# Performance work log

Measured on AMD Instinct MI355X. Metric: run time of the kernel, lower is better.

The kernel has to match this reference:

```python
import jax, jax.numpy as jnp
import numpy as np

NC, S, T, F, D, A = 617, 200000, 15, 5, 64, 768
E, EC, L = 1000000, 20000, 2


def setup_inputs():
    key = jax.random.key(0)
    ks = jax.random.split(key, 24)
    f = jnp.float32
    sc = 0.08
    return {
        "company_ts": jax.random.normal(ks[0], (NC, T, F), f),
        "sentence_x": jax.random.normal(ks[1], (S, A), f),
        "company_ids": jnp.arange(NC, dtype=jnp.int32),
        "ei_c2c_src": jax.random.randint(ks[2], (EC,), 0, NC),
        "ei_c2c_dst": jax.random.randint(ks[3], (EC,), 0, NC),
        "ei_s2c_src": jax.random.randint(ks[4], (E,), 0, S),
        "ei_s2c_dst": jax.random.randint(ks[5], (E,), 0, NC),
        "ei_c2s_src": jax.random.randint(ks[6], (E,), 0, NC),
        "ei_c2s_dst": jax.random.randint(ks[7], (E,), 0, S),
        "bn_gamma": jnp.ones((T,), f),
        "bn_beta": jnp.zeros((T,), f),
        "lstm_Wih0": sc * jax.random.normal(ks[8], (4 * D, 1), f),
        "lstm_Whh0": sc * jax.random.normal(ks[9], (4 * D, D), f),
        "lstm_bih0": jnp.zeros((4 * D,), f),
        "lstm_bhh0": jnp.zeros((4 * D,), f),
        "lstm_Wih1": sc * jax.random.normal(ks[10], (4 * D, D), f),
        "lstm_Whh1": sc * jax.random.normal(ks[11], (4 * D, D), f),
        "lstm_bih1": jnp.zeros((4 * D,), f),
        "lstm_bhh1": jnp.zeros((4 * D,), f),
        "fc_W": sc * jax.random.normal(ks[12], (D, D), f),
        "fc_b": jnp.zeros((D,), f),
        "comp_emb": jax.random.normal(ks[13], (NC, D), f),
        "proj_W": sc * jax.random.normal(ks[14], (D, A), f),
        "proj_b": jnp.zeros((D,), f),
        "gin_W": sc * jax.random.normal(ks[15], (L, 3, D, D), f),
        "gin_b": jnp.zeros((L, 3, D), f),
        "gin_a": 0.25 * jnp.ones((L, 3), f),  # PReLU slope, torch default init
        "cls_W": sc * jax.random.normal(ks[16], (2, D), f),
        "cls_b": jnp.zeros((2,), f),
    }


def _lstm_layer(x, Wih, Whh, bih, bhh):
    # x: [N, T, I] -> [N, T, H]; torch gate order i, f, g, o
    N = x.shape[0]
    H = Whh.shape[1]

    def step(carry, xt):
        h, c = carry
        g = xt @ Wih.T + h @ Whh.T + bih + bhh
        i, fg, gg, o = jnp.split(g, 4, axis=-1)
        c = jax.nn.sigmoid(fg) * c + jax.nn.sigmoid(i) * jnp.tanh(gg)
        h = jax.nn.sigmoid(o) * jnp.tanh(c)
        return (h, c), h

    init = (jnp.zeros((N, H), x.dtype), jnp.zeros((N, H), x.dtype))
    _, hs = jax.lax.scan(step, init, jnp.swapaxes(x, 0, 1))
    return jnp.swapaxes(hs, 0, 1)


def _gin(x_src, x_dst, src, dst, n_dst, W, b, a):
    # GINConv(eps=0), nn = Linear + PReLU: prelu(W @ (x_dst + sum_{e->i} x_src[src_e]) + b)
    msg = jax.ops.segment_sum(x_src[src], dst, num_segments=n_dst)
    h = (x_dst + msg) @ W.T + b
    return jnp.where(h >= 0, h, a * h)


def reference(company_ts, sentence_x, company_ids, ei_c2c_src, ei_c2c_dst,
              ei_s2c_src, ei_s2c_dst, ei_c2s_src, ei_c2s_dst,
              bn_gamma, bn_beta, lstm_Wih0, lstm_Whh0, lstm_bih0, lstm_bhh0,
              lstm_Wih1, lstm_Whh1, lstm_bih1, lstm_bhh1, fc_W, fc_b,
              comp_emb, proj_W, proj_b, gin_W, gin_b, gin_a, cls_W, cls_b):
    # LSTM branch on the second-to-last timeseries feature
    ts = company_ts[:, :, -2:-1]                       # [NC, T, 1]
    mean = ts.mean(axis=(0, 2), keepdims=True)         # BatchNorm1d(T), training stats
    var = ts.var(axis=(0, 2), keepdims=True)
    ts = (ts - mean) / jnp.sqrt(var + 1e-5)
    ts = ts * bn_gamma[None, :, None] + bn_beta[None, :, None]
    h = _lstm_layer(ts, lstm_Wih0, lstm_Whh0, lstm_bih0, lstm_bhh0)
    h = _lstm_layer(h, lstm_Wih1, lstm_Whh1, lstm_bih1, lstm_bhh1)
    comp_ts = jax.nn.relu(h[:, -1, :] @ fc_W.T + fc_b)  # [NC, D]

    # node features: company = lstm + embedding; sentence = projected article emb
    comp = comp_ts + comp_emb[company_ids]
    sent = sentence_x @ proj_W.T + proj_b               # [S, D]

    # to_hetero(GConv): per-edge-type GINConv, sum-aggregate over edge types per dst type
    n_comp, n_sent = comp.shape[0], sent.shape[0]
    for l in range(gin_W.shape[0]):
        new_comp = (_gin(comp, comp, ei_c2c_src, ei_c2c_dst, n_comp,
                         gin_W[l, 0], gin_b[l, 0], gin_a[l, 0])
                    + _gin(sent, comp, ei_s2c_src, ei_s2c_dst, n_comp,
                           gin_W[l, 1], gin_b[l, 1], gin_a[l, 1]))
        new_sent = _gin(comp, sent, ei_c2s_src, ei_c2s_dst, n_sent,
                        gin_W[l, 2], gin_b[l, 2], gin_a[l, 2])
        comp, sent = new_comp, new_sent

    return comp @ cls_W.T + cls_b                       # [NC, 2]
```

## Files before the change

### kernel.cpp

```cpp
#include <hip/hip_runtime.h>

#define NCC 617
#define TTT 15
#define FFF 5
#define SSN 200000
#define EEN 1000000
#define ECN 20000
#define CSBLK 196
#define NB2 512
#define EPB2 ((EEN + NB2 - 1) / NB2)
#define ZN (NCC + NCC + SSN + SSN)

typedef unsigned short u16;
typedef unsigned int   u32;

using short8  = __attribute__((ext_vector_type(8))) short;
using f32x4v  = __attribute__((ext_vector_type(4))) float;

__device__ __forceinline__ float bf2f(u16 u){ return __uint_as_float(((u32)u) << 16); }
__device__ __forceinline__ u16 f2bf(float f){
  u32 x = __float_as_uint(f);
  u32 r = (x + 0x7fffu + ((x >> 16) & 1u)) >> 16;
  return (u16)r;
}
__device__ __forceinline__ u32 pk2(float a, float b){ return (u32)f2bf(a) | ((u32)f2bf(b) << 16); }
__device__ __forceinline__ float sigm(float x){ return 1.0f / (1.0f + __expf(-x)); }

__global__ __launch_bounds__(256) void k_hist2z(const int* __restrict__ dst, int* __restrict__ blockHist,
                                                int* __restrict__ cntBase){
  __shared__ int h[NCC];
  int b = blockIdx.x, tid = threadIdx.x;
  const int zper = (ZN + NB2 - 1) / NB2;
  for (int i = tid; i < zper; i += 256){
    int gi = b * zper + i;
    if (gi < ZN) cntBase[gi] = 0;
  }
  for (int i = tid; i < NCC; i += 256) h[i] = 0;
  __syncthreads();
  int e0 = b * EPB2;
  int e1 = e0 + EPB2; if (e1 > EEN) e1 = EEN;
  for (int e = e0 + tid; e < e1; e += 256) atomicAdd(&h[dst[e]], 1);
  __syncthreads();
  for (int i = tid; i < NCC; i += 256) blockHist[i * NB2 + b] = h[i];
}

__global__ __launch_bounds__(256) void k_hist_all(const int* d1, int n1, int* c1,
                                                  const int* d2, int n2, int* c2){
  int i = blockIdx.x * 256 + threadIdx.x;
  if (i < n1) atomicAdd(&c1[d1[i]], 1);
  else if (i < n1 + n2) atomicAdd(&c2[d2[i - n1]], 1);
}

__global__ __launch_bounds__(64) void k_colscan(int* __restrict__ blockHist, int* __restrict__ colTotal){
  int d = blockIdx.x, lane = threadIdx.x;
  int base = 0;
  for (int j = 0; j < NB2; j += 64){
    int v = blockHist[d * NB2 + j + lane];
    int orig = v;
    #pragma unroll
    for (int s = 1; s < 64; s <<= 1){
      int t = __shfl_up(v, s, 64);
      if (lane >= s) v += t;
    }
    blockHist[d * NB2 + j + lane] = base + v - orig;
    base += __shfl(v, 63, 64);
  }
  if (lane == 0) colTotal[d] = base;
}

__global__ __launch_bounds__(1024) void k_scan2(const int* cntA, int* ofsA,
                                                const int* cntB, int* ofsB, int n){
  __shared__ int buf[1024];
  int t = threadIdx.x;
  for (int pass = 0; pass < 2; ++pass){
    const int* cnt = pass ? cntB : cntA;
    int* ofs = pass ? ofsB : ofsA;
    int v = (t < n) ? cnt[t] : 0;
    buf[t] = v;
    __syncthreads();
    for (int d = 1; d < 1024; d <<= 1){
      int x = (t >= d) ? buf[t - d] : 0;
      __syncthreads();
      buf[t] += x;
      __syncthreads();
    }
    if (t < n) ofs[t] = (t == 0) ? 0 : buf[t - 1];
    if (t == 0) ofs[n] = buf[n - 1];
    __syncthreads();
  }
}

__global__ __launch_bounds__(1024) void k_scan_blocks(const int* cnt, int* ofs, int n, int* bsum){
  __shared__ int buf[1024];
  int t = threadIdx.x;
  int gi = blockIdx.x * 1024 + t;
  int v = (gi < n) ? cnt[gi] : 0;
  buf[t] = v;
  __syncthreads();
  for (int d = 1; d < 1024; d <<= 1){
    int x = (t >= d) ? buf[t - d] : 0;
    __syncthreads();
    buf[t] += x;
    __syncthreads();
  }
  if (gi < n) ofs[gi] = buf[t] - v;
  if (t == 1023) bsum[blockIdx.x] = buf[1023];
}

__global__ __launch_bounds__(1024) void k_scan_addB(int* __restrict__ ofs, const int* __restrict__ bsum, int n){
  __shared__ int sboff[CSBLK + 1];
  int tid = threadIdx.x, lane = tid & 63;
  if (tid < 64){
    int base = 0;
    for (int j = 0; j < CSBLK; j += 64){
      int idx = j + lane;
      int v = (idx < CSBLK) ? bsum[idx] : 0;
      int orig = v;
      #pragma unroll
      for (int s = 1; s < 64; s <<= 1){
        int t2 = __shfl_up(v, s, 64);
        if (lane >= s) v += t2;
      }
      if (idx < CSBLK) sboff[idx] = base + v - orig;
      base += __shfl(v, 63, 64);
    }
    if (lane == 0) sboff[CSBLK] = base;
  }
  __syncthreads();
  int gi = blockIdx.x * 1024 + tid;
  if (gi < n) ofs[gi] += sboff[blockIdx.x];
  if (blockIdx.x == 0 && tid == 0) ofs[n] = sboff[CSBLK];
}

__global__ __launch_bounds__(256) void k_scatter2(const int* __restrict__ src, const int* __restrict__ dst,
                                                  const int* __restrict__ blockHist, const int* __restrict__ off,
                                                  int* __restrict__ bkt){
  __shared__ int cur[NCC];
  int b = blockIdx.x, tid = threadIdx.x;
  for (int i = tid; i < NCC; i += 256) cur[i] = off[i] + blockHist[i * NB2 + b];
  __syncthreads();
  int e0 = b * EPB2;
  int e1 = e0 + EPB2; if (e1 > EEN) e1 = EEN;
  for (int e = e0 + tid; e < e1; e += 256){
    int d = dst[e];
    int p = atomicAdd(&cur[d], 1);
    bkt[p] = src[e];
  }
}

__global__ __launch_bounds__(256) void k_scatter_all(const int* s1, const int* d1, const int* off1, int* cnt1, int* bkt1, int n1,
                                                     const int* s2, const int* d2, const int* off2, int* cnt2, int* bkt2, int n2){
  int i = blockIdx.x * 256 + threadIdx.x;
  if (i < n1){
    int d = d1[i]; int p = off1[d] + atomicAdd(&cnt1[d], 1); bkt1[p] = s1[i];
  } else if (i < n1 + n2){
    int k = i - n1;
    int d = d2[k]; int p = off2[d] + atomicAdd(&cnt2[d], 1); bkt2[p] = s2[k];
  }
}

__global__ __launch_bounds__(256) void k_bn(const float* ts, const float* gamma, const float* beta, float* outp){
  __shared__ float ss[256], s2[256];
  int t = blockIdx.x, tid = threadIdx.x;
  float a = 0.f, b = 0.f;
  for (int c = tid; c < NCC; c += 256){
    float v = ts[(c * TTT + t) * FFF + 3];
    a += v; b += v * v;
  }
  ss[tid] = a; s2[tid] = b;
  __syncthreads();
  for (int d = 128; d > 0; d >>= 1){
    if (tid < d){ ss[tid] += ss[tid + d]; s2[tid] += s2[tid + d]; }
    __syncthreads();
  }
  float mean = ss[0] / (float)NCC;
  float var  = s2[0] / (float)NCC - mean * mean;
  float rstd = rsqrtf(var + 1e-5f);
  float g = gamma[t], be = beta[t];
  for (int c = tid; c < NCC; c += 256){
    float v = ts[(c * TTT + t) * FFF + 3];
    outp[c * TTT + t] = (v - mean) * rstd * g + be;
  }
}

__global__ __launch_bounds__(256) void k_lstm0(const float* tsn, const float* Wih0, const float* Whh0,
                                               const float* bih0, const float* bhh0, float* h0seq){
  __shared__ __align__(16) u16 sW[64 * 256];
  __shared__ float sWi[256];
  __shared__ float sB[256];
  int tid = threadIdx.x;
  for (int i = tid; i < 64 * 256; i += 256){
    int j = i >> 6, k = i & 63;
    sW[k * 256 + j] = f2bf(Whh0[i]);
  }
  if (tid < 256){ sWi[tid] = Wih0[tid]; sB[tid] = bih0[tid] + bhh0[tid]; }
  __syncthreads();
  int wave = tid >> 6, lane = tid & 63;
  int c = blockIdx.x * 4 + wave;
  if (c >= NCC) return;
  float wi_i = sWi[lane], wi_f = sWi[64 + lane], wi_g = sWi[128 + lane], wi_o = sWi[192 + lane];
  float b_i = sB[lane], b_f = sB[64 + lane], b_g = sB[128 + lane], b_o = sB[192 + lane];
  float h = 0.f, cs = 0.f;
  for (int t = 0; t < TTT; ++t){
    float x = tsn[c * TTT + t];
    float gi = b_i + x * wi_i, gf = b_f + x * wi_f, gg = b_g + x * wi_g, go = b_o + x * wi_o;
    #pragma unroll 4
    for (int k = 0; k < 64; ++k){
      float hk = __shfl(h, k, 64);
      const u16* w = &sW[k * 256 + lane];
      gi += hk * bf2f(w[0]);
      gf += hk * bf2f(w[64]);
      gg += hk * bf2f(w[128]);
      go += hk * bf2f(w[192]);
    }
    cs = sigm(gf) * cs + sigm(gi) * tanhf(gg);
    h  = sigm(go) * tanhf(cs);
    h0seq[(c * TTT + t) * 64 + lane] = h;
  }
}

__global__ __launch_bounds__(256, 1) void k_lstm1(const float* h0seq, const float* Wih1, const float* Whh1,
                                                  const float* bih1, const float* bhh1,
                                                  const float* fcW, const float* fcb,
                                                  const float* emb, const int* ids, float* comp0){
  __shared__ __align__(16) u16 sWi[64 * 256];
  __shared__ __align__(16) u16 sWh[64 * 256];
  int tid = threadIdx.x;
  for (int i = tid; i < 64 * 256; i += 256){
    int j = i >> 6, k = i & 63;
    sWi[k * 256 + j] = f2bf(Wih1[i]);
    sWh[k * 256 + j] = f2bf(Whh1[i]);
  }
  __syncthreads();
  int wave = tid >> 6, lane = tid & 63;
  int c = blockIdx.x * 4 + wave;
  int ci = (c < NCC) ? c : (NCC - 1);
  float b_i = bih1[lane]        + bhh1[lane];
  float b_f = bih1[64 + lane]   + bhh1[64 + lane];
  float b_g = bih1[128 + lane]  + bhh1[128 + lane];
  float b_o = bih1[192 + lane]  + bhh1[192 + lane];
  float h = 0.f, cs = 0.f;
  for (int t = 0; t < TTT; ++t){
    float x = h0seq[(ci * TTT + t) * 64 + lane];
    float gi = b_i, gf = b_f, gg = b_g, go = b_o;
    #pragma unroll 4
    for (int k = 0; k < 64; ++k){
      float xk = __shfl(x, k, 64);
      float hk = __shfl(h, k, 64);
      const u16* wi = &sWi[k * 256 + lane];
      const u16* wh = &sWh[k * 256 + lane];
      gi += xk * bf2f(wi[0])   + hk * bf2f(wh[0]);
      gf += xk * bf2f(wi[64])  + hk * bf2f(wh[64]);
      gg += xk * bf2f(wi[128]) + hk * bf2f(wh[128]);
      go += xk * bf2f(wi[192]) + hk * bf2f(wh[192]);
    }
    cs = sigm(gf) * cs + sigm(gi) * tanhf(gg);
    h  = sigm(go) * tanhf(cs);
  }
  __syncthreads();
  float* fws = (float*)sWi;
  for (int i = tid; i < 64 * 64; i += 256){
    int d = i >> 6, k = i & 63;
    fws[k * 64 + d] = fcW[i];
  }
  __syncthreads();
  float y = fcb[lane];
  #pragma unroll 4
  for (int k = 0; k < 64; ++k){
    float hk = __shfl(h, k, 64);
    y += hk * fws[k * 64 + lane];
  }
  y = fmaxf(y, 0.f);
  if (c < NCC) comp0[c * 64 + lane] = y + emb[ids[c] * 64 + lane];
}

__global__ __launch_bounds__(256) void k_projm(const float* __restrict__ A, const float* __restrict__ W,
                                               const float* __restrict__ pb, u16* __restrict__ sent0){
  __shared__ __align__(16) u16 sA[128 * 64];
  __shared__ __align__(16) u16 sB[64 * 64];
  char* sAb = (char*)sA;
  char* sBb = (char*)sB;
  int tid = threadIdx.x;
  int wave = tid >> 6, lane = tid & 63;
  int l15 = lane & 15, lg = lane >> 4;
  int s0 = blockIdx.x * 128;

  int rA = tid >> 1, hA = tid & 1;
  int sA_row = s0 + rA; if (sA_row >= SSN) sA_row = SSN - 1;
  const float* gA0 = &A[(size_t)sA_row * 768 + hA * 32];
  u32 aw_base = (u32)(rA * 128 + hA * 64);
  u32 aw_swz  = (u32)((rA & 7) << 4);
  int nB = tid >> 2, qB = tid & 3;
  const float* gB0 = &W[(size_t)nB * 768 + qB * 16];
  u32 bw_base = (u32)(nB * 128 + qB * 32);
  u32 bw_swz  = (u32)((nB & 7) << 4);

  int arow = wave * 32 + l15;
  u32 ar_swz = (u32)((arow & 7) << 4);
  u32 ar_base = (u32)(arow * 128 + lg * 16);
  u32 br_swz = (u32)((l15 & 7) << 4);
  u32 br_base = (u32)(l15 * 128 + lg * 16);

  f32x4v acc[2][4] = {};

  for (int kc = 0; kc < 12; ++kc){
    __syncthreads();
    {
      const float* g = gA0 + kc * 64;
      #pragma unroll
      for (int q = 0; q < 4; ++q){
        float4 va = ((const float4*)g)[2 * q];
        float4 vb = ((const float4*)g)[2 * q + 1];
        uint4 w;
        w.x = pk2(va.x, va.y); w.y = pk2(va.z, va.w);
        w.z = pk2(vb.x, vb.y); w.w = pk2(vb.z, vb.w);
        *(uint4*)(sAb + ((aw_base + q * 16) ^ aw_swz)) = w;
      }
    }
    {
      const float* g = gB0 + kc * 64;
      #pragma unroll
      for (int q = 0; q < 2; ++q){
        float4 va = ((const float4*)g)[2 * q];
        float4 vb = ((const float4*)g)[2 * q + 1];
        uint4 w;
        w.x = pk2(va.x, va.y); w.y = pk2(va.z, va.w);
        w.z = pk2(vb.x, vb.y); w.w = pk2(vb.z, vb.w);
        *(uint4*)(sBb + ((bw_base + q * 16) ^ bw_swz)) = w;
      }
    }
    __syncthreads();
    #pragma unroll
    for (int ks = 0; ks < 2; ++ks){
      short8 a0 = *(const short8*)(sAb + ((ar_base + 0    + ks * 64) ^ ar_swz));
      short8 a1 = *(const short8*)(sAb + ((ar_base + 2048 + ks * 64) ^ ar_swz));
      short8 b0 = *(const short8*)(sBb + ((br_base + 0    + ks * 64) ^ br_swz));
      short8 b1 = *(const short8*)(sBb + ((br_base + 2048 + ks * 64) ^ br_swz));
      short8 b2 = *(const short8*)(sBb + ((br_base + 4096 + ks * 64) ^ br_swz));
      short8 b3 = *(const short8*)(sBb + ((br_base + 6144 + ks * 64) ^ br_swz));
      acc[0][0] = __builtin_amdgcn_mfma_f32_16x16x32_bf16(a0, b0, acc[0][0], 0, 0, 0);
      acc[0][1] = __builtin_amdgcn_mfma_f32_16x16x32_bf16(a0, b1, acc[0][1], 0, 0, 0);
      acc[0][2] = __builtin_amdgcn_mfma_f32_16x16x32_bf16(a0, b2, acc[0][2], 0, 0, 0);
      acc[0][3] = __builtin_amdgcn_mfma_f32_16x16x32_bf16(a0, b3, acc[0][3], 0, 0, 0);
      acc[1][0] = __builtin_amdgcn_mfma_f32_16x16x32_bf16(a1, b0, acc[1][0], 0, 0, 0);
      acc[1][1] = __builtin_amdgcn_mfma_f32_16x16x32_bf16(a1, b1, acc[1][1], 0, 0, 0);
      acc[1][2] = __builtin_amdgcn_mfma_f32_16x16x32_bf16(a1, b2, acc[1][2], 0, 0, 0);
      acc[1][3] = __builtin_amdgcn_mfma_f32_16x16x32_bf16(a1, b3, acc[1][3], 0, 0, 0);
    }
  }

  float bias[4];
  #pragma unroll
  for (int nt = 0; nt < 4; ++nt) bias[nt] = pb[nt * 16 + l15];
  #pragma unroll
  for (int mt = 0; mt < 2; ++mt){
    #pragma unroll
    for (int j = 0; j < 4; ++j){
      int s = s0 + wave * 32 + mt * 16 + lg * 4 + j;
      if (s < SSN){
        #pragma unroll
        for (int nt = 0; nt < 4; ++nt)
          sent0[(size_t)s * 64 + nt * 16 + l15] = f2bf(acc[mt][nt][j] + bias[nt]);
      }
    }
  }
}

__global__ __launch_bounds__(256) void k_sgin(const u16* __restrict__ sentIn, const float* __restrict__ compIn,
                                              const int* __restrict__ ofs, const int* __restrict__ bkt,
                                              const float* __restrict__ W, const float* __restrict__ b,
                                              const float* __restrict__ aP, u16* __restrict__ sentOut){
  __shared__ __align__(16) float Wt[64 * 68];
  __shared__ __align__(16) float Xt[64 * 68];
  __shared__ int eb[512];
  __shared__ int sofs[65];
  int tid = threadIdx.x;
  for (int i = tid; i < 4096; i += 256){
    int j = i >> 6, k = i & 63;
    Wt[k * 68 + j] = W[i];
  }
  int sBase = blockIdx.x * 64;
  if (tid < 65) sofs[tid] = ofs[sBase + tid];
  __syncthreads();
  int E0 = sofs[0];
  int tot = sofs[64] - E0;
  int staged = tot < 512 ? tot : 512;
  for (int i = tid; i < staged; i += 256) eb[i] = bkt[E0 + i];
  __syncthreads();
  int wave = tid >> 6, lane = tid & 63;
  for (int q = 0; q < 16; ++q){
    int sL = wave * 16 + q;
    int s = sBase + sL;
    float acc = bf2f(sentIn[(size_t)s * 64 + lane]);
    int e0 = sofs[sL], e1 = sofs[sL + 1];
    for (int e = e0; e < e1; ++e){
      int r = e - E0;
      int src = (r < 512) ? eb[r] : bkt[e];
      acc += compIn[src * 64 + lane];
    }
    Xt[lane * 68 + sL] = acc;
  }
  __syncthreads();
  int n0 = (tid & 15) * 4, sG = (tid >> 4) * 4;
  float acc[4][4] = {};
  #pragma unroll 4
  for (int k = 0; k < 64; ++k){
    float4 a4 = *(const float4*)&Xt[k * 68 + sG];
    float4 w4 = *(const float4*)&Wt[k * 68 + n0];
    float a_[4] = {a4.x, a4.y, a4.z, a4.w};
    float w_[4] = {w4.x, w4.y, w4.z, w4.w};
    #pragma unroll
    for (int i = 0; i < 4; ++i)
      #pragma unroll
      for (int j = 0; j < 4; ++j)
        acc[i][j] += a_[i] * w_[j];
  }
  float alpha = *aP;
  float4 bv = *(const float4*)&b[n0];
  float b_[4] = {bv.x, bv.y, bv.z, bv.w};
  __syncthreads();
  #pragma unroll
  for (int i = 0; i < 4; ++i){
    ushort4 o;
    #pragma unroll
    for (int j = 0; j < 4; ++j){
      float h = acc[i][j] + b_[j];
      h = (h >= 0.f) ? h : alpha * h;
      ((u16*)&o)[j] = f2bf(h);
    }
    *(ushort4*)&sentOut[(size_t)(sBase + sG + i) * 64 + n0] = o;
  }
}

__global__ __launch_bounds__(1024) void k_cgin(const float* __restrict__ compIn, const u16* __restrict__ sentIn,
                                               const int* __restrict__ ofsA, const int* __restrict__ bktA,
                                               const int* __restrict__ ofsB, const int* __restrict__ bktB,
                                               const float* __restrict__ Wa, const float* __restrict__ ba, const float* aaP,
                                               const float* __restrict__ Wb, const float* __restrict__ bb, const float* abP,
                                               float* __restrict__ compOut,
                                               const float* __restrict__ clsW, const float* __restrict__ clsb,
                                               float* __restrict__ outp){
  __shared__ __align__(16) float Wat[64 * 68];
  __shared__ __align__(16) float Wbt[64 * 68];
  __shared__ int eidx[2048];
  __shared__ float part[16][2][64];
  __shared__ float xa[64], xb[64], outab[128];
  int tid = threadIdx.x;
  for (int i = tid; i < 4096; i += 1024){
    int j = i >> 6, k = i & 63;
    Wat[k * 68 + j] = Wa[i];
    Wbt[k * 68 + j] = Wb[i];
  }
  int wave = tid >> 6, lane = tid & 63;
  int c = blockIdx.x;
  float accA = 0.f, accB = 0.f;
  int a0 = ofsA[c], a1 = ofsA[c + 1];
  for (int base = a0; base < a1; base += 2048){
    int cnt = a1 - base; if (cnt > 2048) cnt = 2048;
    __syncthreads();
    for (int i = tid; i < cnt; i += 1024) eidx[i] = bktA[base + i];
    __syncthreads();
    for (int i = wave; i < cnt; i += 16) accA += compIn[eidx[i] * 64 + lane];
  }
  int b0 = ofsB[c], b1 = ofsB[c + 1];
  for (int base = b0; base < b1; base += 2048){
    int cnt = b1 - base; if (cnt > 2048) cnt = 2048;
    __syncthreads();
    for (int i = tid; i < cnt; i += 1024) eidx[i] = bktB[base + i];
    __syncthreads();
    #pragma unroll 4
    for (int i = wave; i < cnt; i += 16) accB += bf2f(sentIn[(size_t)eidx[i] * 64 + lane]);
  }
  part[wave][0][lane] = accA;
  part[wave][1][lane] = accB;
  __syncthreads();
  if (tid < 128){
    int l = tid & 63, which = tid >> 6;
    float m = 0.f;
    #pragma unroll
    for (int w = 0; w < 16; ++w) m += part[w][which][l];
    float ci = compIn[c * 64 + l];
    if (which == 0) xa[l] = ci + m; else xb[l] = ci + m;
  }
  __syncthreads();
  if (tid < 128){
    int j = tid & 63;
    const float* X  = (tid < 64) ? xa : xb;
    const float* Wt = (tid < 64) ? Wat : Wbt;
    float acc = (tid < 64) ? ba[j] : bb[j];
    #pragma unroll 4
    for (int k = 0; k < 64; ++k) acc += X[k] * Wt[k * 68 + j];
    float al = (tid < 64) ? *aaP : *abP;
    outab[tid] = (acc >= 0.f) ? acc : al * acc;
  }
  __syncthreads();
  if (clsW){
    if (tid < 64) xa[tid] = outab[tid] + outab[64 + tid];
    __syncthreads();
    if (tid < 128){
      int j = tid >> 6;
      float p = xa[lane] * clsW[j * 64 + lane];
      #pragma unroll
      for (int s = 32; s > 0; s >>= 1) p += __shfl_down(p, s, 64);
      if (lane == 0) outp[c * 2 + j] = p + clsb[j];
    }
  } else {
    if (tid < 64) compOut[c * 64 + tid] = outab[tid] + outab[64 + tid];
  }
}

extern "C" void kernel_launch(void* const* d_in, const int* in_sizes, int n_in,
                              void* d_out, int out_size, void* d_ws, size_t ws_size,
                              hipStream_t stream) {
  (void)in_sizes; (void)n_in; (void)out_size; (void)ws_size;
  const float* company_ts = (const float*)d_in[0];
  const float* sentence_x = (const float*)d_in[1];
  const int*   company_ids = (const int*)d_in[2];
  const int*   c2c_src = (const int*)d_in[3];
  const int*   c2c_dst = (const int*)d_in[4];
  const int*   s2c_src = (const int*)d_in[5];
  const int*   s2c_dst = (const int*)d_in[6];
  const int*   c2s_src = (const int*)d_in[7];
  const int*   c2s_dst = (const int*)d_in[8];
  const float* bn_gamma = (const float*)d_in[9];
  const float* bn_beta  = (const float*)d_in[10];
  const float* Wih0 = (const float*)d_in[11];
  const float* Whh0 = (const float*)d_in[12];
  const float* bih0 = (const float*)d_in[13];
  const float* bhh0 = (const float*)d_in[14];
  const float* Wih1 = (const float*)d_in[15];
  const float* Whh1 = (const float*)d_in[16];
  const float* bih1 = (const float*)d_in[17];
  const float* bhh1 = (const float*)d_in[18];
  const float* fc_W = (const float*)d_in[19];
  const float* fc_b = (const float*)d_in[20];
  const float* comp_emb = (const float*)d_in[21];
  const float* proj_W = (const float*)d_in[22];
  const float* proj_b = (const float*)d_in[23];
  const float* gin_W = (const float*)d_in[24];
  const float* gin_b = (const float*)d_in[25];
  const float* gin_a = (const float*)d_in[26];
  const float* cls_W = (const float*)d_in[27];
  const float* cls_b = (const float*)d_in[28];
  float* outp = (float*)d_out;

  char* ws = (char*)d_ws;
  size_t off = 0;
  auto alloc = [&](size_t bytes)->char* {
    char* r = ws + off;
    off += (bytes + 255) & ~(size_t)255;
    return r;
  };
  float* ts_norm = (float*)alloc((size_t)NCC * TTT * 4);
  float* h0seq   = (float*)alloc((size_t)NCC * TTT * 64 * 4);
  float* comp0   = (float*)alloc((size_t)NCC * 64 * 4);
  float* comp1   = (float*)alloc((size_t)NCC * 64 * 4);
  u16*   sent0   = (u16*)alloc((size_t)SSN * 64 * 2);
  int*   blockHist = (int*)alloc((size_t)NCC * NB2 * 4);
  int*   colTotal  = (int*)alloc((size_t)NCC * 4);
  int*   cnt_c2c  = (int*)alloc((size_t)ZN * 4);
  int*   cnt2_c2c = cnt_c2c + NCC;
  int*   cnt_c2s  = cnt2_c2c + NCC;
  int*   cnt2_c2s = cnt_c2s + SSN;
  int*   off_c2c = (int*)alloc((size_t)(NCC + 1) * 4);
  int*   off_s2c = (int*)alloc((size_t)(NCC + 1) * 4);
  int*   off_c2s = (int*)alloc((size_t)(SSN + 1) * 4);
  int*   bkt_c2c = (int*)alloc((size_t)ECN * 4);
  int*   bkt_s2c = (int*)alloc((size_t)EEN * 4);
  int*   bkt_c2s = (int*)alloc((size_t)EEN * 4);
  int*   bsum    = (int*)alloc(256 * 4);

  k_hist2z<<<NB2, 256, 0, stream>>>(s2c_dst, blockHist, cnt_c2c);
  k_hist_all<<<(ECN + EEN + 255) / 256, 256, 0, stream>>>(c2c_dst, ECN, cnt_c2c, c2s_dst, EEN, cnt_c2s);
  k_colscan<<<NCC, 64, 0, stream>>>(blockHist, colTotal);
  k_scan2<<<1, 1024, 0, stream>>>(cnt_c2c, off_c2c, colTotal, off_s2c, NCC);
  k_scan_blocks<<<CSBLK, 1024, 0, stream>>>(cnt_c2s, off_c2s, SSN, bsum);
  k_scan_addB<<<CSBLK, 1024, 0, stream>>>(off_c2s, bsum, SSN);
  k_scatter2<<<NB2, 256, 0, stream>>>(s2c_src, s2c_dst, blockHist, off_s2c, bkt_s2c);
  k_scatter_all<<<(ECN + EEN + 255) / 256, 256, 0, stream>>>(
      c2c_src, c2c_dst, off_c2c, cnt2_c2c, bkt_c2c, ECN,
      c2s_src, c2s_dst, off_c2s, cnt2_c2s, bkt_c2s, EEN);

  k_bn<<<TTT, 256, 0, stream>>>(company_ts, bn_gamma, bn_beta, ts_norm);
  k_lstm0<<<(NCC + 3) / 4, 256, 0, stream>>>(ts_norm, Wih0, Whh0, bih0, bhh0, h0seq);
  k_lstm1<<<(NCC + 3) / 4, 256, 0, stream>>>(h0seq, Wih1, Whh1, bih1, bhh1, fc_W, fc_b,
                                             comp_emb, company_ids, comp0);

  k_projm<<<(SSN + 127) / 128, 256, 0, stream>>>(sentence_x, proj_W, proj_b, sent0);

  k_cgin<<<NCC, 1024, 0, stream>>>(comp0, sent0,
                                   off_c2c, bkt_c2c, off_s2c, bkt_s2c,
                                   gin_W + 0 * 4096, gin_b + 0 * 64, gin_a + 0,
                                   gin_W + 1 * 4096, gin_b + 1 * 64, gin_a + 1,
                                   comp1, nullptr, nullptr, nullptr);
  k_sgin<<<SSN / 64, 256, 0, stream>>>(sent0, comp0, off_c2s, bkt_c2s,
                                       gin_W + 2 * 4096, gin_b + 2 * 64, gin_a + 2,
                                       sent0 );

  k_cgin<<<NCC, 1024, 0, stream>>>(comp1, sent0,
                                   off_c2c, bkt_c2c, off_s2c, bkt_s2c,
                                   gin_W + 3 * 4096, gin_b + 3 * 64, gin_a + 3,
                                   gin_W + 4 * 4096, gin_b + 4 * 64, gin_a + 4,
                                   nullptr, cls_W, cls_b, outp);
}
```

Baseline: 687.1 us.

## Fuse CSR build kernels, merge LSTM layers, and use MFMA in sentence GIN

Combines the histogram, scan and scatter launches into fewer multi-role kernels and folds batch-norm into a scan kernel, cutting launch count and serialization. Fuses the two LSTM layers into one kernel with gate-interleaved bf16 weights for vector LDS loads, which removes the h0seq round trip through global memory. Replaces the fp32 FMA tile GEMM in the sentence GIN with bf16 MFMA on swizzled LDS. The GIN inputs are now rounded to bf16 before the GEMM, and the fused LSTM kernel needs more LDS per block.

```diff
diff --git a/kernel.cpp b/kernel.cpp
--- a/kernel.cpp
+++ b/kernel.cpp
@@ -10,6 +10,7 @@
 #define NB2 512
 #define EPB2 ((EEN + NB2 - 1) / NB2)
 #define ZN (NCC + NCC + SSN + SSN)
+#define HALLB ((ECN + EEN + 255) / 256)
 
 typedef unsigned short u16;
 typedef unsigned int   u32;
@@ -26,240 +27,239 @@
 __device__ __forceinline__ u32 pk2(float a, float b){ return (u32)f2bf(a) | ((u32)f2bf(b) << 16); }
 __device__ __forceinline__ float sigm(float x){ return 1.0f / (1.0f + __expf(-x)); }
 
-__global__ __launch_bounds__(256) void k_hist2z(const int* __restrict__ dst, int* __restrict__ blockHist,
-                                                int* __restrict__ cntBase){
+__global__ __launch_bounds__(256) void k_zero(int* p, int n){
+  int i = blockIdx.x * 256 + threadIdx.x;
+  if (i < n) p[i] = 0;
+}
+
+__global__ __launch_bounds__(256) void k_histF(const int* __restrict__ s2c_dst, int* __restrict__ blockHist,
+                                               const int* __restrict__ c2c_dst, int* __restrict__ cnt_c2c,
+                                               const int* __restrict__ c2s_dst, int* __restrict__ cnt_c2s){
   __shared__ int h[NCC];
   int b = blockIdx.x, tid = threadIdx.x;
-  const int zper = (ZN + NB2 - 1) / NB2;
-  for (int i = tid; i < zper; i += 256){
-    int gi = b * zper + i;
-    if (gi < ZN) cntBase[gi] = 0;
-  }
-  for (int i = tid; i < NCC; i += 256) h[i] = 0;
-  __syncthreads();
-  int e0 = b * EPB2;
-  int e1 = e0 + EPB2; if (e1 > EEN) e1 = EEN;
-  for (int e = e0 + tid; e < e1; e += 256) atomicAdd(&h[dst[e]], 1);
-  __syncthreads();
-  for (int i = tid; i < NCC; i += 256) blockHist[i * NB2 + b] = h[i];
-}
-
-__global__ __launch_bounds__(256) void k_hist_all(const int* d1, int n1, int* c1,
-                                                  const int* d2, int n2, int* c2){
-  int i = blockIdx.x * 256 + threadIdx.x;
-  if (i < n1) atomicAdd(&c1[d1[i]], 1);
-  else if (i < n1 + n2) atomicAdd(&c2[d2[i - n1]], 1);
-}
-
-__global__ __launch_bounds__(64) void k_colscan(int* __restrict__ blockHist, int* __restrict__ colTotal){
-  int d = blockIdx.x, lane = threadIdx.x;
-  int base = 0;
-  for (int j = 0; j < NB2; j += 64){
-    int v = blockHist[d * NB2 + j + lane];
-    int orig = v;
-    #pragma unroll
-    for (int s = 1; s < 64; s <<= 1){
-      int t = __shfl_up(v, s, 64);
-      if (lane >= s) v += t;
-    }
-    blockHist[d * NB2 + j + lane] = base + v - orig;
-    base += __shfl(v, 63, 64);
-  }
-  if (lane == 0) colTotal[d] = base;
-}
-
-__global__ __launch_bounds__(1024) void k_scan2(const int* cntA, int* ofsA,
-                                                const int* cntB, int* ofsB, int n){
+  if (b < NB2){
+    for (int i = tid; i < NCC; i += 256) h[i] = 0;
+    __syncthreads();
+    int e0 = b * EPB2;
+    int e1 = e0 + EPB2; if (e1 > EEN) e1 = EEN;
+    for (int e = e0 + tid; e < e1; e += 256) atomicAdd(&h[s2c_dst[e]], 1);
+    __syncthreads();
+    for (int i = tid; i < NCC; i += 256) blockHist[i * NB2 + b] = h[i];
+  } else {
+    int i = (b - NB2) * 256 + tid;
+    if (i < ECN) atomicAdd(&cnt_c2c[c2c_dst[i]], 1);
+    else if (i < ECN + EEN) atomicAdd(&cnt_c2s[c2s_dst[i - ECN]], 1);
+  }
+}
+
+__global__ __launch_bounds__(1024) void k_scanA(int* __restrict__ blockHist, int* __restrict__ colTotal,
+                                                const int* __restrict__ cnt_c2s, int* __restrict__ off_c2s,
+                                                int* __restrict__ bsum,
+                                                const float* __restrict__ ts, const float* __restrict__ gamma,
+                                                const float* __restrict__ beta, float* __restrict__ tsn){
   __shared__ int buf[1024];
-  int t = threadIdx.x;
-  for (int pass = 0; pass < 2; ++pass){
-    const int* cnt = pass ? cntB : cntA;
-    int* ofs = pass ? ofsB : ofsA;
-    int v = (t < n) ? cnt[t] : 0;
-    buf[t] = v;
+  __shared__ float ss[1024], s2[1024];
+  int b = blockIdx.x, tid = threadIdx.x;
+  if (b < NCC){
+    if (tid < 64){
+      int lane = tid;
+      int base = 0;
+      for (int j = 0; j < NB2; j += 64){
+        int v = blockHist[b * NB2 + j + lane];
+        int orig = v;
+        #pragma unroll
+        for (int s = 1; s < 64; s <<= 1){
+          int t = __shfl_up(v, s, 64);
+          if (lane >= s) v += t;
+        }
+        blockHist[b * NB2 + j + lane] = base + v - orig;
+        base += __shfl(v, 63, 64);
+      }
+      if (lane == 0) colTotal[b] = base;
+    }
+  } else if (b < NCC + CSBLK) {
+    int bb = b - NCC;
+    int gi = bb * 1024 + tid;
+    int v = (gi < SSN) ? cnt_c2s[gi] : 0;
+    buf[tid] = v;
     __syncthreads();
     for (int d = 1; d < 1024; d <<= 1){
-      int x = (t >= d) ? buf[t - d] : 0;
+      int x = (tid >= d) ? buf[tid - d] : 0;
       __syncthreads();
-      buf[t] += x;
+      buf[tid] += x;
       __syncthreads();
     }
-    if (t < n) ofs[t] = (t == 0) ? 0 : buf[t - 1];
-    if (t == 0) ofs[n] = buf[n - 1];
-    __syncthreads();
-  }
-}
-
-__global__ __launch_bounds__(1024) void k_scan_blocks(const int* cnt, int* ofs, int n, int* bsum){
+    if (gi < SSN) off_c2s[gi] = buf[tid] - v;
+    if (tid == 1023) bsum[bb] = buf[1023];
+  } else {
+    int t = b - (NCC + CSBLK);
+    float a = 0.f, s = 0.f;
+    for (int c = tid; c < NCC; c += 1024){
+      float v = ts[(c * TTT + t) * FFF + 3];
+      a += v; s += v * v;
+    }
+    ss[tid] = a; s2[tid] = s;
+    __syncthreads();
+    for (int d = 512; d > 0; d >>= 1){
+      if (tid < d){ ss[tid] += ss[tid + d]; s2[tid] += s2[tid + d]; }
+      __syncthreads();
+    }
+    float mean = ss[0] / (float)NCC;
+    float var  = s2[0] / (float)NCC - mean * mean;
+    float rstd = rsqrtf(var + 1e-5f);
+    float g = gamma[t], be = beta[t];
+    for (int c = tid; c < NCC; c += 1024){
+      float v = ts[(c * TTT + t) * FFF + 3];
+      tsn[c * TTT + t] = (v - mean) * rstd * g + be;
+    }
+  }
+}
+
+__global__ __launch_bounds__(1024) void k_scanB(const int* __restrict__ cnt_c2c, int* __restrict__ off_c2c,
+                                                const int* __restrict__ colTotal, int* __restrict__ off_s2c,
+                                                int* __restrict__ off_c2s, const int* __restrict__ bsum){
   __shared__ int buf[1024];
-  int t = threadIdx.x;
-  int gi = blockIdx.x * 1024 + t;
-  int v = (gi < n) ? cnt[gi] : 0;
-  buf[t] = v;
-  __syncthreads();
-  for (int d = 1; d < 1024; d <<= 1){
-    int x = (t >= d) ? buf[t - d] : 0;
-    __syncthreads();
-    buf[t] += x;
-    __syncthreads();
-  }
-  if (gi < n) ofs[gi] = buf[t] - v;
-  if (t == 1023) bsum[blockIdx.x] = buf[1023];
-}
-
-__global__ __launch_bounds__(1024) void k_scan_addB(int* __restrict__ ofs, const int* __restrict__ bsum, int n){
   __shared__ int sboff[CSBLK + 1];
-  int tid = threadIdx.x, lane = tid & 63;
-  if (tid < 64){
-    int base = 0;
-    for (int j = 0; j < CSBLK; j += 64){
-      int idx = j + lane;
-      int v = (idx < CSBLK) ? bsum[idx] : 0;
-      int orig = v;
-      #pragma unroll
-      for (int s = 1; s < 64; s <<= 1){
-        int t2 = __shfl_up(v, s, 64);
-        if (lane >= s) v += t2;
+  int b = blockIdx.x, tid = threadIdx.x;
+  if (b == 0){
+    for (int pass = 0; pass < 2; ++pass){
+      const int* cnt = pass ? colTotal : cnt_c2c;
+      int* ofs = pass ? off_s2c : off_c2c;
+      int v = (tid < NCC) ? cnt[tid] : 0;
+      buf[tid] = v;
+      __syncthreads();
+      for (int d = 1; d < 1024; d <<= 1){
+        int x = (tid >= d) ? buf[tid - d] : 0;
+        __syncthreads();
+        buf[tid] += x;
+        __syncthreads();
       }
-      if (idx < CSBLK) sboff[idx] = base + v - orig;
-      base += __shfl(v, 63, 64);
-    }
-    if (lane == 0) sboff[CSBLK] = base;
-  }
-  __syncthreads();
-  int gi = blockIdx.x * 1024 + tid;
-  if (gi < n) ofs[gi] += sboff[blockIdx.x];
-  if (blockIdx.x == 0 && tid == 0) ofs[n] = sboff[CSBLK];
-}
-
-__global__ __launch_bounds__(256) void k_scatter2(const int* __restrict__ src, const int* __restrict__ dst,
-                                                  const int* __restrict__ blockHist, const int* __restrict__ off,
-                                                  int* __restrict__ bkt){
+      if (tid < NCC) ofs[tid] = (tid == 0) ? 0 : buf[tid - 1];
+      if (tid == 0) ofs[NCC] = buf[NCC - 1];
+      __syncthreads();
+    }
+  } else {
+    int bb = b - 1;
+    int lane = tid & 63;
+    if (tid < 64){
+      int base = 0;
+      for (int j = 0; j < CSBLK; j += 64){
+        int idx = j + lane;
+        int v = (idx < CSBLK) ? bsum[idx] : 0;
+        int orig = v;
+        #pragma unroll
+        for (int s = 1; s < 64; s <<= 1){
+          int t2 = __shfl_up(v, s, 64);
+          if (lane >= s) v += t2;
+        }
+        if (idx < CSBLK) sboff[idx] = base + v - orig;
+        base += __shfl(v, 63, 64);
+      }
+      if (lane == 0) sboff[CSBLK] = base;
+    }
+    __syncthreads();
+    int gi = bb * 1024 + tid;
+    if (gi < SSN) off_c2s[gi] += sboff[bb];
+    if (bb == 0 && tid == 0) off_c2s[SSN] = sboff[CSBLK];
+  }
+}
+
+__global__ __launch_bounds__(256) void k_scatF(const int* __restrict__ s2c_src, const int* __restrict__ s2c_dst,
+                                               const int* __restrict__ blockHist, const int* __restrict__ off_s2c,
+                                               int* __restrict__ bkt_s2c,
+                                               const int* __restrict__ c2c_src, const int* __restrict__ c2c_dst,
+                                               const int* __restrict__ off_c2c, int* __restrict__ cnt2_c2c,
+                                               int* __restrict__ bkt_c2c,
+                                               const int* __restrict__ c2s_src, const int* __restrict__ c2s_dst,
+                                               const int* __restrict__ off_c2s, int* __restrict__ cnt2_c2s,
+                                               int* __restrict__ bkt_c2s){
   __shared__ int cur[NCC];
   int b = blockIdx.x, tid = threadIdx.x;
-  for (int i = tid; i < NCC; i += 256) cur[i] = off[i] + blockHist[i * NB2 + b];
-  __syncthreads();
-  int e0 = b * EPB2;
-  int e1 = e0 + EPB2; if (e1 > EEN) e1 = EEN;
-  for (int e = e0 + tid; e < e1; e += 256){
-    int d = dst[e];
-    int p = atomicAdd(&cur[d], 1);
-    bkt[p] = src[e];
-  }
-}
-
-__global__ __launch_bounds__(256) void k_scatter_all(const int* s1, const int* d1, const int* off1, int* cnt1, int* bkt1, int n1,
-                                                     const int* s2, const int* d2, const int* off2, int* cnt2, int* bkt2, int n2){
-  int i = blockIdx.x * 256 + threadIdx.x;
-  if (i < n1){
-    int d = d1[i]; int p = off1[d] + atomicAdd(&cnt1[d], 1); bkt1[p] = s1[i];
-  } else if (i < n1 + n2){
-    int k = i - n1;
-    int d = d2[k]; int p = off2[d] + atomicAdd(&cnt2[d], 1); bkt2[p] = s2[k];
-  }
-}
-
-__global__ __launch_bounds__(256) void k_bn(const float* ts, const float* gamma, const float* beta, float* outp){
-  __shared__ float ss[256], s2[256];
-  int t = blockIdx.x, tid = threadIdx.x;
-  float a = 0.f, b = 0.f;
-  for (int c = tid; c < NCC; c += 256){
-    float v = ts[(c * TTT + t) * FFF + 3];
-    a += v; b += v * v;
-  }
-  ss[tid] = a; s2[tid] = b;
-  __syncthreads();
-  for (int d = 128; d > 0; d >>= 1){
-    if (tid < d){ ss[tid] += ss[tid + d]; s2[tid] += s2[tid + d]; }
-    __syncthreads();
-  }
-  float mean = ss[0] / (float)NCC;
-  float var  = s2[0] / (float)NCC - mean * mean;
-  float rstd = rsqrtf(var + 1e-5f);
-  float g = gamma[t], be = beta[t];
-  for (int c = tid; c < NCC; c += 256){
-    float v = ts[(c * TTT + t) * FFF + 3];
-    outp[c * TTT + t] = (v - mean) * rstd * g + be;
-  }
-}
-
-__global__ __launch_bounds__(256) void k_lstm0(const float* tsn, const float* Wih0, const float* Whh0,
-                                               const float* bih0, const float* bhh0, float* h0seq){
-  __shared__ __align__(16) u16 sW[64 * 256];
+  if (b < NB2){
+    for (int i = tid; i < NCC; i += 256) cur[i] = off_s2c[i] + blockHist[i * NB2 + b];
+    __syncthreads();
+    int e0 = b * EPB2;
+    int e1 = e0 + EPB2; if (e1 > EEN) e1 = EEN;
+    for (int e = e0 + tid; e < e1; e += 256){
+      int d = s2c_dst[e];
+      int p = atomicAdd(&cur[d], 1);
+      bkt_s2c[p] = s2c_src[e];
+    }
+  } else {
+    int i = (b - NB2) * 256 + tid;
+    if (i < ECN){
+      int d = c2c_dst[i]; int p = off_c2c[d] + atomicAdd(&cnt2_c2c[d], 1); bkt_c2c[p] = c2c_src[i];
+    } else if (i < ECN + EEN){
+      int k = i - ECN;
+      int d = c2s_dst[k]; int p = off_c2s[d] + atomicAdd(&cnt2_c2s[d], 1); bkt_c2s[p] = c2s_src[k];
+    }
+  }
+}
+
+__global__ __launch_bounds__(256, 1) void k_lstm01(const float* __restrict__ tsn,
+                                                   const float* __restrict__ Wih0, const float* __restrict__ Whh0,
+                                                   const float* __restrict__ bih0, const float* __restrict__ bhh0,
+                                                   const float* __restrict__ Wih1, const float* __restrict__ Whh1,
+                                                   const float* __restrict__ bih1, const float* __restrict__ bhh1,
+                                                   const float* __restrict__ fcW, const float* __restrict__ fcb,
+                                                   const float* __restrict__ emb, const int* __restrict__ ids,
+                                                   float* __restrict__ comp0){
+  __shared__ __align__(16) u16 sW0[64 * 64 * 4];
+  __shared__ __align__(16) u16 sP1[64 * 64 * 8];
   __shared__ float sWi[256];
-  __shared__ float sB[256];
+  __shared__ float sB0[256];
   int tid = threadIdx.x;
-  for (int i = tid; i < 64 * 256; i += 256){
-    int j = i >> 6, k = i & 63;
-    sW[k * 256 + j] = f2bf(Whh0[i]);
-  }
-  if (tid < 256){ sWi[tid] = Wih0[tid]; sB[tid] = bih0[tid] + bhh0[tid]; }
-  __syncthreads();
-  int wave = tid >> 6, lane = tid & 63;
-  int c = blockIdx.x * 4 + wave;
-  if (c >= NCC) return;
-  float wi_i = sWi[lane], wi_f = sWi[64 + lane], wi_g = sWi[128 + lane], wi_o = sWi[192 + lane];
-  float b_i = sB[lane], b_f = sB[64 + lane], b_g = sB[128 + lane], b_o = sB[192 + lane];
-  float h = 0.f, cs = 0.f;
-  for (int t = 0; t < TTT; ++t){
-    float x = tsn[c * TTT + t];
-    float gi = b_i + x * wi_i, gf = b_f + x * wi_f, gg = b_g + x * wi_g, go = b_o + x * wi_o;
-    #pragma unroll 4
-    for (int k = 0; k < 64; ++k){
-      float hk = __shfl(h, k, 64);
-      const u16* w = &sW[k * 256 + lane];
-      gi += hk * bf2f(w[0]);
-      gf += hk * bf2f(w[64]);
-      gg += hk * bf2f(w[128]);
-      go += hk * bf2f(w[192]);
-    }
-    cs = sigm(gf) * cs + sigm(gi) * tanhf(gg);
-    h  = sigm(go) * tanhf(cs);
-    h0seq[(c * TTT + t) * 64 + lane] = h;
-  }
-}
-
-__global__ __launch_bounds__(256, 1) void k_lstm1(const float* h0seq, const float* Wih1, const float* Whh1,
-                                                  const float* bih1, const float* bhh1,
-                                                  const float* fcW, const float* fcb,
-                                                  const float* emb, const int* ids, float* comp0){
-  __shared__ __align__(16) u16 sWi[64 * 256];
-  __shared__ __align__(16) u16 sWh[64 * 256];
-  int tid = threadIdx.x;
-  for (int i = tid; i < 64 * 256; i += 256){
-    int j = i >> 6, k = i & 63;
-    sWi[k * 256 + j] = f2bf(Wih1[i]);
-    sWh[k * 256 + j] = f2bf(Whh1[i]);
-  }
+  for (int i = tid; i < 16384; i += 256){
+    int k = i >> 8, j = (i >> 2) & 63, g = i & 3;
+    sW0[i] = f2bf(Whh0[(g * 64 + j) * 64 + k]);
+  }
+  for (int i = tid; i < 32768; i += 256){
+    int k = i >> 9, j = (i >> 3) & 63, g = i & 7;
+    float v = (g < 4) ? Wih1[(g * 64 + j) * 64 + k] : Whh1[((g - 4) * 64 + j) * 64 + k];
+    sP1[i] = f2bf(v);
+  }
+  sWi[tid] = Wih0[tid];
+  sB0[tid] = bih0[tid] + bhh0[tid];
   __syncthreads();
   int wave = tid >> 6, lane = tid & 63;
   int c = blockIdx.x * 4 + wave;
   int ci = (c < NCC) ? c : (NCC - 1);
-  float b_i = bih1[lane]        + bhh1[lane];
-  float b_f = bih1[64 + lane]   + bhh1[64 + lane];
-  float b_g = bih1[128 + lane]  + bhh1[128 + lane];
-  float b_o = bih1[192 + lane]  + bhh1[192 + lane];
-  float h = 0.f, cs = 0.f;
+  float wi_i = sWi[lane], wi_f = sWi[64 + lane], wi_g = sWi[128 + lane], wi_o = sWi[192 + lane];
+  float b0i = sB0[lane], b0f = sB0[64 + lane], b0g = sB0[128 + lane], b0o = sB0[192 + lane];
+  float b1i = bih1[lane]       + bhh1[lane];
+  float b1f = bih1[64 + lane]  + bhh1[64 + lane];
+  float b1g = bih1[128 + lane] + bhh1[128 + lane];
+  float b1o = bih1[192 + lane] + bhh1[192 + lane];
+  float h0 = 0.f, c0 = 0.f, h1 = 0.f, c1 = 0.f;
   for (int t = 0; t < TTT; ++t){
-    float x = h0seq[(ci * TTT + t) * 64 + lane];
-    float gi = b_i, gf = b_f, gg = b_g, go = b_o;
+    float x = tsn[ci * TTT + t];
+    float gi = b0i + x * wi_i, gf = b0f + x * wi_f, gg = b0g + x * wi_g, go = b0o + x * wi_o;
     #pragma unroll 4
     for (int k = 0; k < 64; ++k){
-      float xk = __shfl(x, k, 64);
-      float hk = __shfl(h, k, 64);
-      const u16* wi = &sWi[k * 256 + lane];
-      const u16* wh = &sWh[k * 256 + lane];
-      gi += xk * bf2f(wi[0])   + hk * bf2f(wh[0]);
-      gf += xk * bf2f(wi[64])  + hk * bf2f(wh[64]);
-      gg += xk * bf2f(wi[128]) + hk * bf2f(wh[128]);
-      go += xk * bf2f(wi[192]) + hk * bf2f(wh[192]);
-    }
-    cs = sigm(gf) * cs + sigm(gi) * tanhf(gg);
-    h  = sigm(go) * tanhf(cs);
-  }
-  __syncthreads();
-  float* fws = (float*)sWi;
-  for (int i = tid; i < 64 * 64; i += 256){
+      float hk = __shfl(h0, k, 64);
+      ushort4 w = *(const ushort4*)&sW0[(k * 64 + lane) * 4];
+      gi += hk * bf2f(w.x); gf += hk * bf2f(w.y);
+      gg += hk * bf2f(w.z); go += hk * bf2f(w.w);
+    }
+    c0 = sigm(gf) * c0 + sigm(gi) * tanhf(gg);
+    h0 = sigm(go) * tanhf(c0);
+    gi = b1i; gf = b1f; gg = b1g; go = b1o;
+    #pragma unroll 4
+    for (int k = 0; k < 64; ++k){
+      float xk = __shfl(h0, k, 64);
+      float hk = __shfl(h1, k, 64);
+      short8 wv = *(const short8*)&sP1[(k * 64 + lane) * 8];
+      gi += xk * bf2f((u16)wv[0]) + hk * bf2f((u16)wv[4]);
+      gf += xk * bf2f((u16)wv[1]) + hk * bf2f((u16)wv[5]);
+      gg += xk * bf2f((u16)wv[2]) + hk * bf2f((u16)wv[6]);
+      go += xk * bf2f((u16)wv[3]) + hk * bf2f((u16)wv[7]);
+    }
+    c1 = sigm(gf) * c1 + sigm(gi) * tanhf(gg);
+    h1 = sigm(go) * tanhf(c1);
+  }
+  __syncthreads();
+  float* fws = (float*)sW0;
+  for (int i = tid; i < 4096; i += 256){
     int d = i >> 6, k = i & 63;
     fws[k * 64 + d] = fcW[i];
   }
@@ -267,7 +267,7 @@
   float y = fcb[lane];
   #pragma unroll 4
   for (int k = 0; k < 64; ++k){
-    float hk = __shfl(h, k, 64);
+    float hk = __shfl(h1, k, 64);
     y += hk * fws[k * 64 + lane];
   }
   y = fmaxf(y, 0.f);
@@ -370,14 +370,27 @@
                                               const int* __restrict__ ofs, const int* __restrict__ bkt,
                                               const float* __restrict__ W, const float* __restrict__ b,
                                               const float* __restrict__ aP, u16* __restrict__ sentOut){
-  __shared__ __align__(16) float Wt[64 * 68];
-  __shared__ __align__(16) float Xt[64 * 68];
+  __shared__ __align__(16) u16 sX[64 * 64];
+  __shared__ __align__(16) u16 sW[64 * 64];
   __shared__ int eb[512];
   __shared__ int sofs[65];
+  char* sXb = (char*)sX;
+  char* sWb = (char*)sW;
   int tid = threadIdx.x;
-  for (int i = tid; i < 4096; i += 256){
-    int j = i >> 6, k = i & 63;
-    Wt[k * 68 + j] = W[i];
+  {
+    int n = tid >> 2, q = tid & 3;
+    const float* g = &W[n * 64 + q * 16];
+    u32 wbase = (u32)(n * 128 + q * 32);
+    u32 wswz  = (u32)((n & 7) << 4);
+    #pragma unroll
+    for (int hh = 0; hh < 2; ++hh){
+      float4 va = ((const float4*)g)[2 * hh];
+      float4 vb = ((const float4*)g)[2 * hh + 1];
+      uint4 w;
+      w.x = pk2(va.x, va.y); w.y = pk2(va.z, va.w);
+      w.z = pk2(vb.x, vb.y); w.w = pk2(vb.z, vb.w);
+      *(uint4*)(sWb + ((wbase + hh * 16) ^ wswz)) = w;
+    }
   }
   int sBase = blockIdx.x * 64;
   if (tid < 65) sofs[tid] = ofs[sBase + tid];
@@ -398,37 +411,34 @@
       int src = (r < 512) ? eb[r] : bkt[e];
       acc += compIn[src * 64 + lane];
     }
-    Xt[lane * 68 + sL] = acc;
-  }
-  __syncthreads();
-  int n0 = (tid & 15) * 4, sG = (tid >> 4) * 4;
-  float acc[4][4] = {};
-  #pragma unroll 4
-  for (int k = 0; k < 64; ++k){
-    float4 a4 = *(const float4*)&Xt[k * 68 + sG];
-    float4 w4 = *(const float4*)&Wt[k * 68 + n0];
-    float a_[4] = {a4.x, a4.y, a4.z, a4.w};
-    float w_[4] = {w4.x, w4.y, w4.z, w4.w};
+    *(u16*)(sXb + (((u32)(sL * 128 + lane * 2)) ^ ((u32)((sL & 7) << 4)))) = f2bf(acc);
+  }
+  __syncthreads();
+  int l15 = lane & 15, lg = lane >> 4;
+  int arow = wave * 16 + l15;
+  u32 ar_swz = (u32)((arow & 7) << 4);
+  u32 br_swz = (u32)((l15 & 7) << 4);
+  f32x4v acc4[4] = {};
+  #pragma unroll
+  for (int ks = 0; ks < 2; ++ks){
+    short8 a0 = *(const short8*)(sXb + (((u32)(arow * 128 + ks * 64 + lg * 16)) ^ ar_swz));
     #pragma unroll
-    for (int i = 0; i < 4; ++i)
-      #pragma unroll
-      for (int j = 0; j < 4; ++j)
-        acc[i][j] += a_[i] * w_[j];
+    for (int nt = 0; nt < 4; ++nt){
+      short8 b0 = *(const short8*)(sWb + (((u32)((nt * 16 + l15) * 128 + ks * 64 + lg * 16)) ^ br_swz));
+      acc4[nt] = __builtin_amdgcn_mfma_f32_16x16x32_bf16(a0, b0, acc4[nt], 0, 0, 0);
+    }
   }
   float alpha = *aP;
-  float4 bv = *(const float4*)&b[n0];
-  float b_[4] = {bv.x, bv.y, bv.z, bv.w};
-  __syncthreads();
   #pragma unroll
-  for (int i = 0; i < 4; ++i){
-    ushort4 o;
+  for (int nt = 0; nt < 4; ++nt){
+    float bb = b[nt * 16 + l15];
     #pragma unroll
     for (int j = 0; j < 4; ++j){
-      float h = acc[i][j] + b_[j];
+      int srow = sBase + wave * 16 + lg * 4 + j;
+      float h = acc4[nt][j] + bb;
       h = (h >= 0.f) ? h : alpha * h;
-      ((u16*)&o)[j] = f2bf(h);
-    }
-    *(ushort4*)&sentOut[(size_t)(sBase + sG + i) * 64 + n0] = o;
+      sentOut[(size_t)srow * 64 + nt * 16 + l15] = f2bf(h);
+    }
   }
 }
 
@@ -552,7 +562,6 @@
     return r;
   };
   float* ts_norm = (float*)alloc((size_t)NCC * TTT * 4);
-  float* h0seq   = (float*)alloc((size_t)NCC * TTT * 64 * 4);
   float* comp0   = (float*)alloc((size_t)NCC * 64 * 4);
   float* comp1   = (float*)alloc((size_t)NCC * 64 * 4);
   u16*   sent0   = (u16*)alloc((size_t)SSN * 64 * 2);
@@ -570,21 +579,18 @@
   int*   bkt_c2s = (int*)alloc((size_t)EEN * 4);
   int*   bsum    = (int*)alloc(256 * 4);
 
-  k_hist2z<<<NB2, 256, 0, stream>>>(s2c_dst, blockHist, cnt_c2c);
-  k_hist_all<<<(ECN + EEN + 255) / 256, 256, 0, stream>>>(c2c_dst, ECN, cnt_c2c, c2s_dst, EEN, cnt_c2s);
-  k_colscan<<<NCC, 64, 0, stream>>>(blockHist, colTotal);
-  k_scan2<<<1, 1024, 0, stream>>>(cnt_c2c, off_c2c, colTotal, off_s2c, NCC);
-  k_scan_blocks<<<CSBLK, 1024, 0, stream>>>(cnt_c2s, off_c2s, SSN, bsum);
-  k_scan_addB<<<CSBLK, 1024, 0, stream>>>(off_c2s, bsum, SSN);
-  k_scatter2<<<NB2, 256, 0, stream>>>(s2c_src, s2c_dst, blockHist, off_s2c, bkt_s2c);
-  k_scatter_all<<<(ECN + EEN + 255) / 256, 256, 0, stream>>>(
-      c2c_src, c2c_dst, off_c2c, cnt2_c2c, bkt_c2c, ECN,
-      c2s_src, c2s_dst, off_c2s, cnt2_c2s, bkt_c2s, EEN);
-
-  k_bn<<<TTT, 256, 0, stream>>>(company_ts, bn_gamma, bn_beta, ts_norm);
-  k_lstm0<<<(NCC + 3) / 4, 256, 0, stream>>>(ts_norm, Wih0, Whh0, bih0, bhh0, h0seq);
-  k_lstm1<<<(NCC + 3) / 4, 256, 0, stream>>>(h0seq, Wih1, Whh1, bih1, bhh1, fc_W, fc_b,
-                                             comp_emb, company_ids, comp0);
+  k_zero<<<(ZN + 255) / 256, 256, 0, stream>>>(cnt_c2c, ZN);
+  k_histF<<<NB2 + HALLB, 256, 0, stream>>>(s2c_dst, blockHist, c2c_dst, cnt_c2c, c2s_dst, cnt_c2s);
+  k_scanA<<<NCC + CSBLK + TTT, 1024, 0, stream>>>(blockHist, colTotal, cnt_c2s, off_c2s, bsum,
+                                                  company_ts, bn_gamma, bn_beta, ts_norm);
+  k_scanB<<<1 + CSBLK, 1024, 0, stream>>>(cnt_c2c, off_c2c, colTotal, off_s2c, off_c2s, bsum);
+  k_scatF<<<NB2 + HALLB, 256, 0, stream>>>(s2c_src, s2c_dst, blockHist, off_s2c, bkt_s2c,
+                                           c2c_src, c2c_dst, off_c2c, cnt2_c2c, bkt_c2c,
+                                           c2s_src, c2s_dst, off_c2s, cnt2_c2s, bkt_c2s);
+
+  k_lstm01<<<(NCC + 3) / 4, 256, 0, stream>>>(ts_norm, Wih0, Whh0, bih0, bhh0,
+                                              Wih1, Whh1, bih1, bhh1,
+                                              fc_W, fc_b, comp_emb, company_ids, comp0);
 
   k_projm<<<(SSN + 127) / 128, 256, 0, stream>>>(sentence_x, proj_W, proj_b, sent0);
 
```

Result: faster. 565.3 us (-17.7%).
